# Optimization experiments

Hardware: AMD Instinct MI355X
Metric: run time of the kernel (lower is better)

The kernel has to match this reference:

```python
import jax, jax.numpy as jnp
import numpy as np

GRID = 128
DIMS = [64 + 3, 128, 64, 32, 1]  # MLP channel stack from source


def setup_inputs() -> dict:
    key = jax.random.key(0)
    ks = jax.random.split(key, 1 + 2 * (len(DIMS) - 1))
    B = 1
    inp = {"x": jax.random.normal(ks[0], (B, 64, 1, 1), dtype=jnp.float32)}
    for i in range(len(DIMS) - 1):
        cin, cout = DIMS[i], DIMS[i + 1]
        scale = 1.0 / np.sqrt(cin)
        inp[f"W{i+1}"] = jax.random.uniform(ks[1 + 2 * i], (cout, cin), jnp.float32, -scale, scale)
        inp[f"b{i+1}"] = jax.random.uniform(ks[2 + 2 * i], (cout,), jnp.float32, -scale, scale)
    return inp


def _forward(x, W1, b1, W2, b2, W3, b3, W4, b4):
    B = x.shape[0]
    dt = x.dtype
    lines = jnp.linspace(-1.0, 1.0, GRID, dtype=dt)
    a, b, c = jnp.meshgrid(lines, lines, lines, indexing="ij")  # torch default 'ij'
    pts = jnp.stack([a, b, c], axis=0).reshape(3, -1)           # [3, N], N = 128^3
    N = pts.shape[1]
    # broadcast latent over all grid points and concat coords -> [B, 67, N]
    f = jnp.concatenate(
        [jnp.broadcast_to(x.reshape(B, 64, 1), (B, 64, N)),
         jnp.broadcast_to(pts[None], (B, 3, N))],
        axis=1,
    )
    h = jax.nn.relu(jnp.einsum("oc,bcn->bon", W1, f) + b1[:, None])
    h = jax.nn.relu(jnp.einsum("oc,bcn->bon", W2, h) + b2[:, None])
    h = jax.nn.relu(jnp.einsum("oc,bcn->bon", W3, h) + b3[:, None])
    sdf = jax.nn.sigmoid(jnp.einsum("oc,bcn->bon", W4, h) + b4[:, None])  # [B,1,N]
    return sdf.reshape(B, GRID, GRID, GRID)


def reference(x, W1, b1, W2, b2, W3, b3, W4, b4):
    return _forward(x, W1, b1, W2, b2, W3, b3, W4, b4)
```

## Files before the change

kernel.cpp:

```cpp
#include <hip/hip_runtime.h>
#include <hip/hip_bf16.h>
#include <hip/hip_fp16.h>


#define NPTS (128 * 128 * 128)

typedef float f32x4_t __attribute__((ext_vector_type(4)));
typedef float f32x2_t __attribute__((ext_vector_type(2)));
typedef __fp16 g16x2_t __attribute__((ext_vector_type(2)));
typedef _Float16 h16x8_t __attribute__((ext_vector_type(8)));

__device__ __forceinline__ unsigned h2u(g16x2_t h) {
    unsigned u;
    __builtin_memcpy(&u, &h, 4);
    return u;
}
__device__ __forceinline__ g16x2_t u2h(unsigned u) {
    g16x2_t h;
    __builtin_memcpy(&h, &u, 4);
    return h;
}

__global__ __launch_bounds__(256, 2) void mlp_kernel(
    const float* __restrict__ x,  const float* __restrict__ W1,
    const float* __restrict__ b1, const float* __restrict__ W2,
    const float* __restrict__ b2, const float* __restrict__ W3,
    const float* __restrict__ b3, const float* __restrict__ W4,
    const float* __restrict__ b4, float* __restrict__ out) {
    __shared__ __align__(16) unsigned s_basep[16][64];
    __shared__ __align__(16) unsigned s_wcp[64];
    __shared__ __align__(16) float s_b2[64];
    __shared__ __align__(16) float s_b3[32];
    __shared__ __align__(16) float s_w4[32];
    __shared__ __align__(16) unsigned short s_u[13312];

    const int t = threadIdx.x;
    const int w = t >> 6;
    const int lane = t & 63;
    const int quad = lane >> 4;
    const int l15 = lane & 15;
    const float step = 2.0f / 127.0f;

    {
        const int p = t & 63, h = t >> 6;
        const float* r0 = W1 + (2 * p) * 67 + h * 16;
        const float* r1 = r0 + 67;
        const float* xh = x + h * 16;
        float s0 = 0.0f, s1 = 0.0f;
#pragma unroll
        for (int c = 0; c < 16; ++c) {
            const float xc = xh[c];
            s0 = fmaf(r0[c], xc, s0);
            s1 = fmaf(r1[c], xc, s1);
        }
        float2* psum = (float2*)&s_u[10240];
        psum[h * 64 + p] = make_float2(s0, s1);
    }
    const float2* W2v = (const float2*)W2;
#pragma unroll
    for (int it = 0; it < 16; ++it) {
        int pidx = t + 256 * it;
        int idx2 = pidx * 2;
        int o = idx2 >> 7, k = idx2 & 127;
        int mt = o >> 4, lm = o & 15;
        int kb = k >> 5, q = (k >> 3) & 3, jj = k & 7;
        float2 v = W2v[pidx];
        *(unsigned*)&s_u[(mt * 4 + kb) * 512 + (q * 16 + lm) * 8 + jj] =
            h2u(__builtin_amdgcn_cvt_pkrtz(v.x, v.y));
    }
    const float2* W3v = (const float2*)W3;
#pragma unroll
    for (int it = 0; it < 4; ++it) {
        int pidx = t + 256 * it;
        int idx2 = pidx * 2;
        int o = idx2 >> 6, k = idx2 & 63;
        int mt = o >> 4, lm = o & 15;
        int kb = k >> 5, q = (k >> 3) & 3, jj = k & 7;
        float2 v = W3v[pidx];
        *(unsigned*)&s_u[8192 + (mt * 2 + kb) * 512 + (q * 16 + lm) * 8 + jj] =
            h2u(__builtin_amdgcn_cvt_pkrtz(v.x, v.y));
    }
    if (t < 64) s_b2[t] = b2[t];
    if (t < 32) {
        s_b3[t] = b3[t];
        s_w4[t] = W4[t];
    }
    const float bias4 = b4[0];
    __syncthreads();

    if (t < 64) {
        const float2* psum = (const float2*)&s_u[10240];
        float2 q0 = psum[t], q1 = psum[64 + t], q2 = psum[128 + t], q3 = psum[192 + t];
        float s0 = b1[2 * t] + (q0.x + q1.x) + (q2.x + q3.x);
        float s1 = b1[2 * t + 1] + (q0.y + q1.y) + (q2.y + q3.y);
        const float* r0 = W1 + (2 * t) * 67;
        const float* r1 = r0 + 67;
        const float pa = -1.0f + step * (float)(blockIdx.x >> 3);
        const float base0 = fmaf(r0[64], pa, s0);
        const float base1 = fmaf(r1[64], pa, s1);
        const float wb0 = r0[65], wb1 = r1[65];
        const int gj0 = (blockIdx.x & 7) * 16;
        s_wcp[t] = h2u(__builtin_amdgcn_cvt_pkrtz(r0[66], r1[66]));
#pragma unroll
        for (int j = 0; j < 16; ++j) {
            const float pb = -1.0f + step * (float)(gj0 + j);
            s_basep[j][t] = h2u(__builtin_amdgcn_cvt_pkrtz(
                fmaf(wb0, pb, base0), fmaf(wb1, pb, base1)));
        }
    }
    __syncthreads();

    h16x8_t a2[16];
#pragma unroll
    for (int f = 0; f < 16; ++f) a2[f] = *(const h16x8_t*)&s_u[f * 512 + lane * 8];
    h16x8_t a3[4];
#pragma unroll
    for (int f = 0; f < 4; ++f) a3[f] = *(const h16x8_t*)&s_u[8192 + f * 512 + lane * 8];
    f32x4_t b2q[4];
#pragma unroll
    for (int mt = 0; mt < 4; ++mt) b2q[mt] = *(const f32x4_t*)&s_b2[mt * 16 + quad * 4];
    f32x4_t b3q[2];
    f32x2_t w4lo[2], w4hi[2];
#pragma unroll
    for (int mt = 0; mt < 2; ++mt) {
        b3q[mt] = *(const f32x4_t*)&s_b3[mt * 16 + quad * 4];
        float4 wq = *(const float4*)&s_w4[mt * 16 + quad * 4];
        w4lo[mt][0] = wq.x; w4lo[mt][1] = wq.y;
        w4hi[mt][0] = wq.z; w4hi[mt][1] = wq.w;
    }
    unsigned twp[16];
#pragma unroll
    for (int kb = 0; kb < 4; ++kb) {
        uint4 v = *(const uint4*)&s_wcp[kb * 16 + quad * 4];
        twp[kb * 4 + 0] = v.x; twp[kb * 4 + 1] = v.y;
        twp[kb * 4 + 2] = v.z; twp[kb * 4 + 3] = v.w;
    }
#pragma unroll
    for (int i = 0; i < 16; ++i) asm volatile("" : "+v"(twp[i]));
    __syncthreads();

    const int sw = (l15 & 1) * 32;
    unsigned short* h2w = &s_u[w * 2 * 1152];
    float* zf = (float*)&s_u[9216];
    const f32x2_t zero2 = {0.0f, 0.0f};
    const g16x2_t zero2h = {(__fp16)0.0f, (__fp16)0.0f};
    const int outbase = blockIdx.x * 2048 + w * 512;

    auto bphase = [&](int pg, h16x8_t b3f0, h16x8_t b3f1) {
        f32x2_t z2 = zero2;
#pragma unroll
        for (int mt = 0; mt < 2; ++mt) {
            f32x4_t c = b3q[mt];
            c = __builtin_amdgcn_mfma_f32_16x16x32_f16(a3[mt * 2 + 0], b3f0, c, 0, 0, 0);
            c = __builtin_amdgcn_mfma_f32_16x16x32_f16(a3[mt * 2 + 1], b3f1, c, 0, 0, 0);
            f32x2_t h01 = __builtin_elementwise_max((f32x2_t){c[0], c[1]}, zero2);
            f32x2_t h23 = __builtin_elementwise_max((f32x2_t){c[2], c[3]}, zero2);
            z2 = __builtin_elementwise_fma(w4lo[mt], h01, z2);
            z2 = __builtin_elementwise_fma(w4hi[mt], h23, z2);
        }
        zf[w * 512 + (pg & 7) * 64 + l15 * 4 + quad] = z2[0] + z2[1];
    };
    auto cphase = [&](int batch) {
#pragma unroll
        for (int half = 0; half < 2; ++half) {
            const int p = lane + 64 * half;
            const int pg = p >> 4, i = p & 15;
            float4 v = *(const float4*)&zf[w * 512 + pg * 64 + i * 4];
            float z = (v.x + v.y) + (v.z + v.w) + bias4;
            out[outbase + batch * 128 + p] = 1.0f / (1.0f + __expf(-z));
        }
    };

    for (int jrow = 0; jrow < 4; ++jrow) {
        const unsigned* bp = &s_basep[w * 4 + jrow][0];
        unsigned tbp[16];
#pragma unroll
        for (int kb = 0; kb < 4; ++kb) {
            uint4 v = *(const uint4*)&bp[kb * 16 + quad * 4];
            tbp[kb * 4 + 0] = v.x; tbp[kb * 4 + 1] = v.y;
            tbp[kb * 4 + 2] = v.z; tbp[kb * 4 + 3] = v.w;
        }
#pragma unroll
        for (int i = 0; i < 16; ++i) asm volatile("" : "+v"(tbp[i]));

#pragma unroll 2
        for (int pg = 0; pg < 8; ++pg) {
            const int ng = jrow * 8 + pg;
            h16x8_t b3f0, b3f1;
            if (ng > 0) {
                const unsigned short* pslot = h2w + ((ng - 1) & 1) * 1152 + l15 * 72;
                b3f0 = *(const h16x8_t*)&pslot[(0 ^ sw) + quad * 8];
                b3f1 = *(const h16x8_t*)&pslot[(32 ^ sw) + quad * 8];
            }

            const float pc = fmaf(step, (float)((pg * 16) + l15), -1.0f);
            const g16x2_t pc2 = __builtin_amdgcn_cvt_pkrtz(pc, pc);

            h16x8_t bfrag[4];
#pragma unroll
            for (int kb = 0; kb < 4; ++kb) {
                union { h16x8_t v; g16x2_t h[4]; } bb;
#pragma unroll
                for (int p = 0; p < 4; ++p) {
                    g16x2_t hh = __builtin_elementwise_fma(
                        u2h(twp[kb * 4 + p]), pc2, u2h(tbp[kb * 4 + p]));
                    bb.h[p] = __builtin_elementwise_max(hh, zero2h);
                }
                bfrag[kb] = bb.v;
            }
            f32x4_t acc2[4];
#pragma unroll
            for (int mt = 0; mt < 4; ++mt) {
                f32x4_t c = b2q[mt];
#pragma unroll
                for (int kb = 0; kb < 4; ++kb)
                    c = __builtin_amdgcn_mfma_f32_16x16x32_f16(a2[mt * 4 + kb], bfrag[kb], c, 0, 0, 0);
                acc2[mt] = c;
            }
            unsigned short* slot = h2w + (ng & 1) * 1152 + l15 * 72;
#pragma unroll
            for (int mt = 0; mt < 4; ++mt) {
                g16x2_t lo = __builtin_elementwise_max(
                    __builtin_amdgcn_cvt_pkrtz(acc2[mt][0], acc2[mt][1]), zero2h);
                g16x2_t hi = __builtin_elementwise_max(
                    __builtin_amdgcn_cvt_pkrtz(acc2[mt][2], acc2[mt][3]), zero2h);
                uint2 pk;
                pk.x = h2u(lo);
                pk.y = h2u(hi);
                *(uint2*)&slot[(mt * 16 + quad * 4) ^ sw] = pk;
            }
            if (ng > 0) {
                bphase(ng - 1, b3f0, b3f1);
                if (((ng - 1) & 7) == 7) cphase((ng - 1) >> 3);
            }
        }
    }
    {
        const unsigned short* pslot = h2w + (31 & 1) * 1152 + l15 * 72;
        h16x8_t b3f0 = *(const h16x8_t*)&pslot[(0 ^ sw) + quad * 8];
        h16x8_t b3f1 = *(const h16x8_t*)&pslot[(32 ^ sw) + quad * 8];
        bphase(31, b3f0, b3f1);
        cphase(3);
    }
}

extern "C" void kernel_launch(void* const* d_in, const int* in_sizes, int n_in,
                              void* d_out, int out_size, void* d_ws, size_t ws_size,
                              hipStream_t stream) {
    mlp_kernel<<<NPTS / 2048, 256, 0, stream>>>(
        (const float*)d_in[0], (const float*)d_in[1], (const float*)d_in[2],
        (const float*)d_in[3], (const float*)d_in[4], (const float*)d_in[5],
        (const float*)d_in[6], (const float*)d_in[7], (const float*)d_in[8],
        (float*)d_out);
}
```

Baseline: 113.9 us.

## Replace LDS staging of layer-2 activations with permlane swaps

The layer-2 outputs are no longer written to shared memory and read back as layer-3 MFMA B fragments. They are rearranged directly in registers with v_permlane32_swap and v_permlane16_swap. The final cross-quad reduction of the layer-4 dot product also moves from an LDS buffer to permlane swaps, so the one-step software pipeline and the batched sigmoid output phase go away. Output stores become 16 floats per wave per point group instead of 128-wide batches, and LDS use shrinks. This removes LDS traffic and waits, but also removes the overlap between layer 2 of one group and layer 3 of the previous group.

```diff
diff --git a/kernel.cpp b/kernel.cpp
--- a/kernel.cpp
+++ b/kernel.cpp
@@ -9,6 +9,7 @@
 typedef float f32x2_t __attribute__((ext_vector_type(2)));
 typedef __fp16 g16x2_t __attribute__((ext_vector_type(2)));
 typedef _Float16 h16x8_t __attribute__((ext_vector_type(8)));
+typedef unsigned u32x2_t __attribute__((ext_vector_type(2)));
 
 __device__ __forceinline__ unsigned h2u(g16x2_t h) {
     unsigned u;
@@ -19,6 +20,25 @@
     g16x2_t h;
     __builtin_memcpy(&h, &u, 4);
     return h;
+}
+
+__device__ __forceinline__ void pl32_swap(unsigned& a, unsigned& b) {
+#if __has_builtin(__builtin_amdgcn_permlane32_swap)
+    u32x2_t r = __builtin_amdgcn_permlane32_swap(a, b, false, false);
+    a = r[0];
+    b = r[1];
+#else
+    asm("v_permlane32_swap_b32 %0, %1" : "+v"(a), "+v"(b));
+#endif
+}
+__device__ __forceinline__ void pl16_swap(unsigned& a, unsigned& b) {
+#if __has_builtin(__builtin_amdgcn_permlane16_swap)
+    u32x2_t r = __builtin_amdgcn_permlane16_swap(a, b, false, false);
+    a = r[0];
+    b = r[1];
+#else
+    asm("v_permlane16_swap_b32 %0, %1" : "+v"(a), "+v"(b));
+#endif
 }
 
 __global__ __launch_bounds__(256, 2) void mlp_kernel(
@@ -32,7 +52,7 @@
     __shared__ __align__(16) float s_b2[64];
     __shared__ __align__(16) float s_b3[32];
     __shared__ __align__(16) float s_w4[32];
-    __shared__ __align__(16) unsigned short s_u[13312];
+    __shared__ __align__(16) unsigned short s_u[11264];
 
     const int t = threadIdx.x;
     const int w = t >> 6;
@@ -137,39 +157,10 @@
     }
 #pragma unroll
     for (int i = 0; i < 16; ++i) asm volatile("" : "+v"(twp[i]));
-    __syncthreads();
-
-    const int sw = (l15 & 1) * 32;
-    unsigned short* h2w = &s_u[w * 2 * 1152];
-    float* zf = (float*)&s_u[9216];
+
     const f32x2_t zero2 = {0.0f, 0.0f};
     const g16x2_t zero2h = {(__fp16)0.0f, (__fp16)0.0f};
     const int outbase = blockIdx.x * 2048 + w * 512;
-
-    auto bphase = [&](int pg, h16x8_t b3f0, h16x8_t b3f1) {
-        f32x2_t z2 = zero2;
-#pragma unroll
-        for (int mt = 0; mt < 2; ++mt) {
-            f32x4_t c = b3q[mt];
-            c = __builtin_amdgcn_mfma_f32_16x16x32_f16(a3[mt * 2 + 0], b3f0, c, 0, 0, 0);
-            c = __builtin_amdgcn_mfma_f32_16x16x32_f16(a3[mt * 2 + 1], b3f1, c, 0, 0, 0);
-            f32x2_t h01 = __builtin_elementwise_max((f32x2_t){c[0], c[1]}, zero2);
-            f32x2_t h23 = __builtin_elementwise_max((f32x2_t){c[2], c[3]}, zero2);
-            z2 = __builtin_elementwise_fma(w4lo[mt], h01, z2);
-            z2 = __builtin_elementwise_fma(w4hi[mt], h23, z2);
-        }
-        zf[w * 512 + (pg & 7) * 64 + l15 * 4 + quad] = z2[0] + z2[1];
-    };
-    auto cphase = [&](int batch) {
-#pragma unroll
-        for (int half = 0; half < 2; ++half) {
-            const int p = lane + 64 * half;
-            const int pg = p >> 4, i = p & 15;
-            float4 v = *(const float4*)&zf[w * 512 + pg * 64 + i * 4];
-            float z = (v.x + v.y) + (v.z + v.w) + bias4;
-            out[outbase + batch * 128 + p] = 1.0f / (1.0f + __expf(-z));
-        }
-    };
 
     for (int jrow = 0; jrow < 4; ++jrow) {
         const unsigned* bp = &s_basep[w * 4 + jrow][0];
@@ -186,13 +177,6 @@
 #pragma unroll 2
         for (int pg = 0; pg < 8; ++pg) {
             const int ng = jrow * 8 + pg;
-            h16x8_t b3f0, b3f1;
-            if (ng > 0) {
-                const unsigned short* pslot = h2w + ((ng - 1) & 1) * 1152 + l15 * 72;
-                b3f0 = *(const h16x8_t*)&pslot[(0 ^ sw) + quad * 8];
-                b3f1 = *(const h16x8_t*)&pslot[(32 ^ sw) + quad * 8];
-            }
-
             const float pc = fmaf(step, (float)((pg * 16) + l15), -1.0f);
             const g16x2_t pc2 = __builtin_amdgcn_cvt_pkrtz(pc, pc);
 
@@ -217,30 +201,49 @@
                     c = __builtin_amdgcn_mfma_f32_16x16x32_f16(a2[mt * 4 + kb], bfrag[kb], c, 0, 0, 0);
                 acc2[mt] = c;
             }
-            unsigned short* slot = h2w + (ng & 1) * 1152 + l15 * 72;
+            unsigned u[4][2];
 #pragma unroll
             for (int mt = 0; mt < 4; ++mt) {
-                g16x2_t lo = __builtin_elementwise_max(
-                    __builtin_amdgcn_cvt_pkrtz(acc2[mt][0], acc2[mt][1]), zero2h);
-                g16x2_t hi = __builtin_elementwise_max(
-                    __builtin_amdgcn_cvt_pkrtz(acc2[mt][2], acc2[mt][3]), zero2h);
-                uint2 pk;
-                pk.x = h2u(lo);
-                pk.y = h2u(hi);
-                *(uint2*)&slot[(mt * 16 + quad * 4) ^ sw] = pk;
-            }
-            if (ng > 0) {
-                bphase(ng - 1, b3f0, b3f1);
-                if (((ng - 1) & 7) == 7) cphase((ng - 1) >> 3);
-            }
-        }
-    }
-    {
-        const unsigned short* pslot = h2w + (31 & 1) * 1152 + l15 * 72;
-        h16x8_t b3f0 = *(const h16x8_t*)&pslot[(0 ^ sw) + quad * 8];
-        h16x8_t b3f1 = *(const h16x8_t*)&pslot[(32 ^ sw) + quad * 8];
-        bphase(31, b3f0, b3f1);
-        cphase(3);
+                u[mt][0] = h2u(__builtin_elementwise_max(
+                    __builtin_amdgcn_cvt_pkrtz(acc2[mt][0], acc2[mt][1]), zero2h));
+                u[mt][1] = h2u(__builtin_elementwise_max(
+                    __builtin_amdgcn_cvt_pkrtz(acc2[mt][2], acc2[mt][3]), zero2h));
+            }
+            h16x8_t b3f[2];
+#pragma unroll
+            for (int kb = 0; kb < 2; ++kb) {
+                union { h16x8_t v; unsigned wd[4]; } fb;
+#pragma unroll
+                for (int s = 0; s < 2; ++s) {
+                    unsigned A = u[2 * kb][s], B = u[2 * kb + 1][s];
+                    pl32_swap(A, B);
+                    pl16_swap(A, B);
+                    fb.wd[s] = A;
+                    fb.wd[2 + s] = B;
+                }
+                b3f[kb] = fb.v;
+            }
+            f32x2_t z2 = zero2;
+#pragma unroll
+            for (int mt = 0; mt < 2; ++mt) {
+                f32x4_t c = b3q[mt];
+                c = __builtin_amdgcn_mfma_f32_16x16x32_f16(a3[mt * 2 + 0], b3f[0], c, 0, 0, 0);
+                c = __builtin_amdgcn_mfma_f32_16x16x32_f16(a3[mt * 2 + 1], b3f[1], c, 0, 0, 0);
+                f32x2_t h01 = __builtin_elementwise_max((f32x2_t){c[0], c[1]}, zero2);
+                f32x2_t h23 = __builtin_elementwise_max((f32x2_t){c[2], c[3]}, zero2);
+                z2 = __builtin_elementwise_fma(w4lo[mt], h01, z2);
+                z2 = __builtin_elementwise_fma(w4hi[mt], h23, z2);
+            }
+            float z = z2[0] + z2[1];
+            unsigned za = __builtin_bit_cast(unsigned, z), zb = za;
+            pl16_swap(za, zb);
+            z = __builtin_bit_cast(float, za) + __builtin_bit_cast(float, zb);
+            za = __builtin_bit_cast(unsigned, z); zb = za;
+            pl32_swap(za, zb);
+            z = __builtin_bit_cast(float, za) + __builtin_bit_cast(float, zb) + bias4;
+            const float r = 1.0f / (1.0f + __expf(-z));
+            if (quad == 0) out[outbase + ng * 16 + l15] = r;
+        }
     }
 }
 
```

Result: no change. 116.2 us (+2.0%).

## Double per-block work and pipeline two point-groups per iteration with 4-slot buffer

Applied to the files above, without the earlier changes.

Each block now handles 4096 points (32 j-rows) instead of 2048, which halves the grid and amortizes the per-block setup (W1 partial sums, W2/W3 fragment staging). The inner loop processes two 16-point groups per iteration. Layer-2 MFMAs for both are issued before the layer-3 phase of groups from two steps earlier, using a 4-slot LDS ring. The aim is more independent MFMA work to hide latency, at the cost of more LDS (which may lower occupancy), more registers, and fewer blocks (512) across the CUs.

```diff
diff --git a/kernel.cpp b/kernel.cpp
--- a/kernel.cpp
+++ b/kernel.cpp
@@ -27,12 +27,12 @@
     const float* __restrict__ b2, const float* __restrict__ W3,
     const float* __restrict__ b3, const float* __restrict__ W4,
     const float* __restrict__ b4, float* __restrict__ out) {
-    __shared__ __align__(16) unsigned s_basep[16][64];
+    __shared__ __align__(16) unsigned s_basep[32][64];
     __shared__ __align__(16) unsigned s_wcp[64];
     __shared__ __align__(16) float s_b2[64];
     __shared__ __align__(16) float s_b3[32];
     __shared__ __align__(16) float s_w4[32];
-    __shared__ __align__(16) unsigned short s_u[13312];
+    __shared__ __align__(16) unsigned short s_u[22528];
 
     const int t = threadIdx.x;
     const int w = t >> 6;
@@ -95,14 +95,14 @@
         float s1 = b1[2 * t + 1] + (q0.y + q1.y) + (q2.y + q3.y);
         const float* r0 = W1 + (2 * t) * 67;
         const float* r1 = r0 + 67;
-        const float pa = -1.0f + step * (float)(blockIdx.x >> 3);
+        const float pa = -1.0f + step * (float)(blockIdx.x >> 2);
         const float base0 = fmaf(r0[64], pa, s0);
         const float base1 = fmaf(r1[64], pa, s1);
         const float wb0 = r0[65], wb1 = r1[65];
-        const int gj0 = (blockIdx.x & 7) * 16;
+        const int gj0 = (blockIdx.x & 3) * 32;
         s_wcp[t] = h2u(__builtin_amdgcn_cvt_pkrtz(r0[66], r1[66]));
 #pragma unroll
-        for (int j = 0; j < 16; ++j) {
+        for (int j = 0; j < 32; ++j) {
             const float pb = -1.0f + step * (float)(gj0 + j);
             s_basep[j][t] = h2u(__builtin_amdgcn_cvt_pkrtz(
                 fmaf(wb0, pb, base0), fmaf(wb1, pb, base1)));
@@ -140,11 +140,11 @@
     __syncthreads();
 
     const int sw = (l15 & 1) * 32;
-    unsigned short* h2w = &s_u[w * 2 * 1152];
-    float* zf = (float*)&s_u[9216];
+    unsigned short* h2w = &s_u[w * 4608];
+    float* zf = (float*)&s_u[18432];
     const f32x2_t zero2 = {0.0f, 0.0f};
     const g16x2_t zero2h = {(__fp16)0.0f, (__fp16)0.0f};
-    const int outbase = blockIdx.x * 2048 + w * 512;
+    const int outbase = blockIdx.x * 4096 + w * 1024;
 
     auto bphase = [&](int pg, h16x8_t b3f0, h16x8_t b3f1) {
         f32x2_t z2 = zero2;
@@ -170,10 +170,48 @@
             out[outbase + batch * 128 + p] = 1.0f / (1.0f + __expf(-z));
         }
     };
-
-    for (int jrow = 0; jrow < 4; ++jrow) {
-        const unsigned* bp = &s_basep[w * 4 + jrow][0];
-        unsigned tbp[16];
+    unsigned tbp[16];
+    auto aphase = [&](int pgk, f32x4_t acc[4]) {
+        const float pc = fmaf(step, (float)((pgk * 16) + l15), -1.0f);
+        const g16x2_t pc2 = __builtin_amdgcn_cvt_pkrtz(pc, pc);
+        h16x8_t bfrag[4];
+#pragma unroll
+        for (int kb = 0; kb < 4; ++kb) {
+            union { h16x8_t v; g16x2_t h[4]; } bb;
+#pragma unroll
+            for (int p = 0; p < 4; ++p) {
+                g16x2_t hh = __builtin_elementwise_fma(
+                    u2h(twp[kb * 4 + p]), pc2, u2h(tbp[kb * 4 + p]));
+                bb.h[p] = __builtin_elementwise_max(hh, zero2h);
+            }
+            bfrag[kb] = bb.v;
+        }
+#pragma unroll
+        for (int mt = 0; mt < 4; ++mt) {
+            f32x4_t c = b2q[mt];
+#pragma unroll
+            for (int kb = 0; kb < 4; ++kb)
+                c = __builtin_amdgcn_mfma_f32_16x16x32_f16(a2[mt * 4 + kb], bfrag[kb], c, 0, 0, 0);
+            acc[mt] = c;
+        }
+    };
+    auto a3store = [&](int ng, const f32x4_t acc[4]) {
+        unsigned short* slot = h2w + (ng & 3) * 1152 + l15 * 72;
+#pragma unroll
+        for (int mt = 0; mt < 4; ++mt) {
+            g16x2_t lo = __builtin_elementwise_max(
+                __builtin_amdgcn_cvt_pkrtz(acc[mt][0], acc[mt][1]), zero2h);
+            g16x2_t hi = __builtin_elementwise_max(
+                __builtin_amdgcn_cvt_pkrtz(acc[mt][2], acc[mt][3]), zero2h);
+            uint2 pk;
+            pk.x = h2u(lo);
+            pk.y = h2u(hi);
+            *(uint2*)&slot[(mt * 16 + quad * 4) ^ sw] = pk;
+        }
+    };
+
+    for (int jr = 0; jr < 8; ++jr) {
+        const unsigned* bp = &s_basep[w * 8 + jr][0];
 #pragma unroll
         for (int kb = 0; kb < 4; ++kb) {
             uint4 v = *(const uint4*)&bp[kb * 16 + quad * 4];
@@ -184,70 +222,47 @@
         for (int i = 0; i < 16; ++i) asm volatile("" : "+v"(tbp[i]));
 
 #pragma unroll 2
-        for (int pg = 0; pg < 8; ++pg) {
-            const int ng = jrow * 8 + pg;
-            h16x8_t b3f0, b3f1;
-            if (ng > 0) {
-                const unsigned short* pslot = h2w + ((ng - 1) & 1) * 1152 + l15 * 72;
-                b3f0 = *(const h16x8_t*)&pslot[(0 ^ sw) + quad * 8];
-                b3f1 = *(const h16x8_t*)&pslot[(32 ^ sw) + quad * 8];
+        for (int pgp = 0; pgp < 4; ++pgp) {
+            const int pgX = 2 * pgp, pgY = pgX + 1;
+            const int ngX = jr * 8 + pgX, ngY = ngX + 1;
+            h16x8_t bxf0, bxf1, byf0, byf1;
+            if (ngX > 1) {
+                const unsigned short* ps0 = h2w + ((ngX - 2) & 3) * 1152 + l15 * 72;
+                bxf0 = *(const h16x8_t*)&ps0[(0 ^ sw) + quad * 8];
+                bxf1 = *(const h16x8_t*)&ps0[(32 ^ sw) + quad * 8];
+                const unsigned short* ps1 = h2w + ((ngY - 2) & 3) * 1152 + l15 * 72;
+                byf0 = *(const h16x8_t*)&ps1[(0 ^ sw) + quad * 8];
+                byf1 = *(const h16x8_t*)&ps1[(32 ^ sw) + quad * 8];
             }
-
-            const float pc = fmaf(step, (float)((pg * 16) + l15), -1.0f);
-            const g16x2_t pc2 = __builtin_amdgcn_cvt_pkrtz(pc, pc);
-
-            h16x8_t bfrag[4];
-#pragma unroll
-            for (int kb = 0; kb < 4; ++kb) {
-                union { h16x8_t v; g16x2_t h[4]; } bb;
-#pragma unroll
-                for (int p = 0; p < 4; ++p) {
-                    g16x2_t hh = __builtin_elementwise_fma(
-                        u2h(twp[kb * 4 + p]), pc2, u2h(tbp[kb * 4 + p]));
-                    bb.h[p] = __builtin_elementwise_max(hh, zero2h);
-                }
-                bfrag[kb] = bb.v;
+            f32x4_t accX[4], accY[4];
+            aphase(pgX, accX);
+            aphase(pgY, accY);
+            a3store(ngX, accX);
+            a3store(ngY, accY);
+            if (ngX > 1) {
+                bphase(ngX - 2, bxf0, bxf1);
+                bphase(ngY - 2, byf0, byf1);
+                if (((ngY - 2) & 7) == 7) cphase((ngY - 2) >> 3);
             }
-            f32x4_t acc2[4];
-#pragma unroll
-            for (int mt = 0; mt < 4; ++mt) {
-                f32x4_t c = b2q[mt];
-#pragma unroll
-                for (int kb = 0; kb < 4; ++kb)
-                    c = __builtin_amdgcn_mfma_f32_16x16x32_f16(a2[mt * 4 + kb], bfrag[kb], c, 0, 0, 0);
-                acc2[mt] = c;
-            }
-            unsigned short* slot = h2w + (ng & 1) * 1152 + l15 * 72;
-#pragma unroll
-            for (int mt = 0; mt < 4; ++mt) {
-                g16x2_t lo = __builtin_elementwise_max(
-                    __builtin_amdgcn_cvt_pkrtz(acc2[mt][0], acc2[mt][1]), zero2h);
-                g16x2_t hi = __builtin_elementwise_max(
-                    __builtin_amdgcn_cvt_pkrtz(acc2[mt][2], acc2[mt][3]), zero2h);
-                uint2 pk;
-                pk.x = h2u(lo);
-                pk.y = h2u(hi);
-                *(uint2*)&slot[(mt * 16 + quad * 4) ^ sw] = pk;
-            }
-            if (ng > 0) {
-                bphase(ng - 1, b3f0, b3f1);
-                if (((ng - 1) & 7) == 7) cphase((ng - 1) >> 3);
-            }
         }
     }
     {
-        const unsigned short* pslot = h2w + (31 & 1) * 1152 + l15 * 72;
-        h16x8_t b3f0 = *(const h16x8_t*)&pslot[(0 ^ sw) + quad * 8];
-        h16x8_t b3f1 = *(const h16x8_t*)&pslot[(32 ^ sw) + quad * 8];
-        bphase(31, b3f0, b3f1);
-        cphase(3);
+        const unsigned short* ps0 = h2w + (62 & 3) * 1152 + l15 * 72;
+        h16x8_t bxf0 = *(const h16x8_t*)&ps0[(0 ^ sw) + quad * 8];
+        h16x8_t bxf1 = *(const h16x8_t*)&ps0[(32 ^ sw) + quad * 8];
+        const unsigned short* ps1 = h2w + (63 & 3) * 1152 + l15 * 72;
+        h16x8_t byf0 = *(const h16x8_t*)&ps1[(0 ^ sw) + quad * 8];
+        h16x8_t byf1 = *(const h16x8_t*)&ps1[(32 ^ sw) + quad * 8];
+        bphase(62, bxf0, bxf1);
+        bphase(63, byf0, byf1);
+        cphase(7);
     }
 }
 
 extern "C" void kernel_launch(void* const* d_in, const int* in_sizes, int n_in,
                               void* d_out, int out_size, void* d_ws, size_t ws_size,
                               hipStream_t stream) {
-    mlp_kernel<<<NPTS / 2048, 256, 0, stream>>>(
+    mlp_kernel<<<NPTS / 4096, 256, 0, stream>>>(
         (const float*)d_in[0], (const float*)d_in[1], (const float*)d_in[2],
         (const float*)d_in[3], (const float*)d_in[4], (const float*)d_in[5],
         (const float*)d_in[6], (const float*)d_in[7], (const float*)d_in[8],
```

Result: no change. 112.9 us (-0.9%).
